# Kernel optimization log

Hardware: AMD Instinct MI355X
Metric: run time of the kernel (lower is better)

Reference implementation:

```python
import jax, jax.numpy as jnp
import numpy as np

GROUP_SIZE = 64

def _dequant(wq, scale, zero):
    # HQQ groupwise dequant: W = (Wq - zero) * scale, groups along input dim.
    out_dim, in_dim = wq.shape
    g = in_dim // GROUP_SIZE
    w = (wq.astype(jnp.float32).reshape(out_dim, g, GROUP_SIZE) - zero[:, :, None]) * scale[:, :, None]
    return w.reshape(out_dim, in_dim)

def setup_inputs() -> dict:
    key = jax.random.key(0)
    ks = jax.random.split(key, 10)
    T, H, I = 256, 4096, 14336
    G1, G2 = H // GROUP_SIZE, I // GROUP_SIZE  # 64, 224
    x = jax.random.normal(ks[0], (T, H), dtype=jnp.float32)
    w1_q = jax.random.randint(ks[1], (I, H), 0, 16, dtype=jnp.int32)
    w1_scale = jax.random.uniform(ks[2], (I, G1), dtype=jnp.float32) * 0.02
    w1_zero = jax.random.uniform(ks[3], (I, G1), dtype=jnp.float32) * 8.0
    w3_q = jax.random.randint(ks[4], (I, H), 0, 16, dtype=jnp.int32)
    w3_scale = jax.random.uniform(ks[5], (I, G1), dtype=jnp.float32) * 0.02
    w3_zero = jax.random.uniform(ks[6], (I, G1), dtype=jnp.float32) * 8.0
    w2_q = jax.random.randint(ks[7], (H, I), 0, 16, dtype=jnp.int32)
    w2_scale = jax.random.uniform(ks[8], (H, G2), dtype=jnp.float32) * 0.02
    w2_zero = jax.random.uniform(ks[9], (H, G2), dtype=jnp.float32) * 8.0
    return {"x": x, "w1_q": w1_q, "w1_scale": w1_scale, "w1_zero": w1_zero,
            "w3_q": w3_q, "w3_scale": w3_scale, "w3_zero": w3_zero,
            "w2_q": w2_q, "w2_scale": w2_scale, "w2_zero": w2_zero}

def reference(x, w1_q, w1_scale, w1_zero, w3_q, w3_scale, w3_zero, w2_q, w2_scale, w2_zero):
    w1 = _dequant(w1_q, w1_scale, w1_zero)  # [I, H]
    w3 = _dequant(w3_q, w3_scale, w3_zero)  # [I, H]
    w2 = _dequant(w2_q, w2_scale, w2_zero)  # [H, I]
    gate = jax.nn.silu(jnp.einsum('th,ih->ti', x, w1))  # [T, I]
    up = jnp.einsum('th,ih->ti', x, w3)                 # [T, I]
    return jnp.einsum('ti,hi->th', gate * up, w2)       # [T, H]
```

## Files before the change

### kernel.cpp

```cpp
#include <hip/hip_runtime.h>
#include <cstdint>
#include <cstddef>

#define T_DIM 256
#define H_DIM 4096
#define I_DIM 14336

typedef __attribute__((ext_vector_type(8))) short s8v;
typedef __attribute__((ext_vector_type(4))) float f4v;

static constexpr size_t XS_BYTES   = (size_t)T_DIM * H_DIM * 2;
static constexpr size_t ACT_OFF    = XS_BYTES;
static constexpr size_t ACT_BYTES  = (size_t)T_DIM * I_DIM * 2;
static constexpr size_t PART_OFF   = ACT_OFF + ACT_BYTES;
static constexpr size_t PART_BYTES = 8ull * T_DIM * H_DIM * 4;
static constexpr size_t WS_NEEDED  = PART_OFF + PART_BYTES;

__device__ __forceinline__ unsigned short f2bf(float f) {
    unsigned u = __builtin_bit_cast(unsigned, f);
    u += 0x7fffu + ((u >> 16) & 1u);
    return (unsigned short)(u >> 16);
}

__device__ __forceinline__ void g2lds16(const void* g, void* l) {
    __builtin_amdgcn_global_load_lds(
        (const __attribute__((address_space(1))) unsigned int*)g,
        (__attribute__((address_space(3))) unsigned int*)l,
        16, 0, 0);
}

__device__ __forceinline__ s8v dq8(const int4 qa, const int4 qb, float s, float ns) {
    union { unsigned short u[8]; s8v v; } r;
    r.u[0] = f2bf(fmaf((float)qa.x, s, ns));
    r.u[1] = f2bf(fmaf((float)qa.y, s, ns));
    r.u[2] = f2bf(fmaf((float)qa.z, s, ns));
    r.u[3] = f2bf(fmaf((float)qa.w, s, ns));
    r.u[4] = f2bf(fmaf((float)qb.x, s, ns));
    r.u[5] = f2bf(fmaf((float)qb.y, s, ns));
    r.u[6] = f2bf(fmaf((float)qb.z, s, ns));
    r.u[7] = f2bf(fmaf((float)qb.w, s, ns));
    return r.v;
}

__global__ __launch_bounds__(256) void k_prep(const float* __restrict__ x,
                                              unsigned short* __restrict__ xs) {
    int gs   = blockIdx.x * 256 + threadIdx.x;
    int kt   = gs >> 11;
    int rem  = gs & 2047;
    int row  = rem >> 3;
    int slot = rem & 7;
    const float* xp = x + (size_t)row * H_DIM + kt * 64 + slot * 8;
    float4 a = *(const float4*)xp;
    float4 b = *(const float4*)(xp + 4);
    union { unsigned short u[8]; s8v v; } r;
    r.u[0] = f2bf(a.x); r.u[1] = f2bf(a.y); r.u[2] = f2bf(a.z); r.u[3] = f2bf(a.w);
    r.u[4] = f2bf(b.x); r.u[5] = f2bf(b.y); r.u[6] = f2bf(b.z); r.u[7] = f2bf(b.w);
    size_t di = (size_t)kt * 16384 + (size_t)row * 64 + (size_t)((slot ^ (row & 7)) * 8);
    *(s8v*)(xs + di) = r.v;
}

__global__ __launch_bounds__(512, 2) void k_gemm1(
    const int* __restrict__ w1q, const float* __restrict__ w1s, const float* __restrict__ w1z,
    const int* __restrict__ w3q, const float* __restrict__ w3s, const float* __restrict__ w3z,
    const unsigned short* __restrict__ xs, unsigned short* __restrict__ act)
{
    __shared__ unsigned char lds[49152];
    const int tid  = threadIdx.x;
    const int blk  = blockIdx.x;
    const int n0   = blk * 64;
    const int wid  = tid >> 6;
    const int lane = tid & 63;
    const int wr   = wid >> 1;
    const int wc   = wid & 1;
    const int lr   = lane & 15;
    const int lkb  = lane >> 4;
    const int aswz = (lr & 7) << 4;

    const int srow  = tid >> 3;
    const int sslot = tid & 7;
    const size_t grow = (size_t)(n0 + srow) * H_DIM + (size_t)sslot * 8;
    const int wbyte = srow * 128 + ((sslot * 16) ^ ((srow & 7) << 4));
    const float* s1p = w1s + (size_t)(n0 + srow) * 64;
    const float* z1p = w1z + (size_t)(n0 + srow) * 64;
    const float* s3p = w3s + (size_t)(n0 + srow) * 64;
    const float* z3p = w3z + (size_t)(n0 + srow) * 64;

    f4v accg[4][2], accu[4][2];
    const f4v fz = {0.f, 0.f, 0.f, 0.f};
    #pragma unroll
    for (int i = 0; i < 4; ++i)
        #pragma unroll
        for (int j = 0; j < 2; ++j) { accg[i][j] = fz; accu[i][j] = fz; }

    const unsigned char* xsb = (const unsigned char*)xs;

    for (int kt = 0; kt < 64; ++kt) {
        {
            const unsigned char* gsrc = xsb + (size_t)kt * 32768 + (size_t)wid * 1024
                                            + (size_t)lane * 16;
            unsigned char* ldst = lds + wid * 1024;
            #pragma unroll
            for (int j = 0; j < 4; ++j)
                g2lds16(gsrc + j * 8192, ldst + j * 8192);
        }
        {
            const int4* p1 = (const int4*)(w1q + grow + (size_t)kt * 64);
            const int4* p3 = (const int4*)(w3q + grow + (size_t)kt * 64);
            int4 q1a = p1[0], q1b = p1[1];
            int4 q3a = p3[0], q3b = p3[1];
            float s1 = s1p[kt]; float ns1 = -z1p[kt] * s1;
            float s3 = s3p[kt]; float ns3 = -z3p[kt] * s3;
            *(s8v*)(lds + 32768 + wbyte) = dq8(q1a, q1b, s1, ns1);
            *(s8v*)(lds + 40960 + wbyte) = dq8(q3a, q3b, s3, ns3);
        }
        __syncthreads();
        #pragma unroll
        for (int kf = 0; kf < 2; ++kf) {
            const int kb = (kf * 64 + lkb * 16) ^ aswz;
            s8v a[4];
            #pragma unroll
            for (int mf = 0; mf < 4; ++mf)
                a[mf] = *(const s8v*)(lds + (wr * 64 + mf * 16 + lr) * 128 + kb);
            s8v b1[2], b3[2];
            #pragma unroll
            for (int nf = 0; nf < 2; ++nf) {
                const int rbo = (wc * 32 + nf * 16 + lr) * 128 + kb;
                b1[nf] = *(const s8v*)(lds + 32768 + rbo);
                b3[nf] = *(const s8v*)(lds + 40960 + rbo);
            }
            #pragma unroll
            for (int mf = 0; mf < 4; ++mf)
                #pragma unroll
                for (int nf = 0; nf < 2; ++nf) {
                    accg[mf][nf] = __builtin_amdgcn_mfma_f32_16x16x32_bf16(a[mf], b1[nf], accg[mf][nf], 0, 0, 0);
                    accu[mf][nf] = __builtin_amdgcn_mfma_f32_16x16x32_bf16(a[mf], b3[nf], accu[mf][nf], 0, 0, 0);
                }
        }
        __syncthreads();
    }

    unsigned char* actb = (unsigned char*)act + (size_t)blk * 32768;
    #pragma unroll
    for (int mf = 0; mf < 4; ++mf)
        #pragma unroll
        for (int nf = 0; nf < 2; ++nf)
            #pragma unroll
            for (int r = 0; r < 4; ++r) {
                const int m  = wr * 64 + mf * 16 + lkb * 4 + r;
                const int nl = wc * 32 + nf * 16 + lr;
                float g = accg[mf][nf][r];
                float u = accu[mf][nf][r];
                float sg = g / (1.0f + __expf(-g));
                *(unsigned short*)(actb + ((m * 128 + nl * 2) ^ ((m & 7) << 4))) = f2bf(sg * u);
            }
}

template<bool ATOMIC>
__global__ __launch_bounds__(512, 2) void k_gemm2(
    const int* __restrict__ w2q, const float* __restrict__ w2s, const float* __restrict__ w2z,
    const unsigned short* __restrict__ act, float* __restrict__ outp)
{
    __shared__ unsigned char lds[49152];
    const int tid  = threadIdx.x;
    const int nb   = blockIdx.x & 31;
    const int kc   = blockIdx.x >> 5;
    const int n0   = nb * 128;
    const int wid  = tid >> 6;
    const int lane = tid & 63;
    const int wr   = wid >> 2;
    const int wc   = wid & 3;
    const int lr   = lane & 15;
    const int lkb  = lane >> 4;
    const int aswz = (lr & 7) << 4;

    const int srow = tid >> 2;
    const int ss2  = (tid & 3) * 2;
    const size_t grow = (size_t)(n0 + srow) * I_DIM + (size_t)ss2 * 8;
    const int wb0 = srow * 128 + ((ss2 * 16)       ^ ((srow & 7) << 4));
    const int wb1 = srow * 128 + (((ss2 + 1) * 16) ^ ((srow & 7) << 4));
    const float* s2p = w2s + (size_t)(n0 + srow) * 224;
    const float* z2p = w2z + (size_t)(n0 + srow) * 224;

    f4v acc[8][2];
    const f4v fz = {0.f, 0.f, 0.f, 0.f};
    #pragma unroll
    for (int i = 0; i < 8; ++i) { acc[i][0] = fz; acc[i][1] = fz; }

    const unsigned char* actb = (const unsigned char*)act;
    const int kt0 = kc * 28;

    for (int kk = 0; kk < 28; ++kk) {
        const int kt = kt0 + kk;
        {
            const unsigned char* gsrc = actb + (size_t)kt * 32768 + (size_t)wid * 1024
                                             + (size_t)lane * 16;
            unsigned char* ldst = lds + wid * 1024;
            #pragma unroll
            for (int j = 0; j < 4; ++j)
                g2lds16(gsrc + j * 8192, ldst + j * 8192);
        }
        {
            const int4* p2 = (const int4*)(w2q + grow + (size_t)kt * 64);
            int4 qa = p2[0], qb = p2[1], qc = p2[2], qd = p2[3];
            float s2 = s2p[kt]; float ns2 = -z2p[kt] * s2;
            *(s8v*)(lds + 32768 + wb0) = dq8(qa, qb, s2, ns2);
            *(s8v*)(lds + 32768 + wb1) = dq8(qc, qd, s2, ns2);
        }
        __syncthreads();
        #pragma unroll
        for (int kf = 0; kf < 2; ++kf) {
            const int kb = (kf * 64 + lkb * 16) ^ aswz;
            s8v b2[2];
            #pragma unroll
            for (int nf = 0; nf < 2; ++nf)
                b2[nf] = *(const s8v*)(lds + 32768 + (wc * 32 + nf * 16 + lr) * 128 + kb);
            #pragma unroll
            for (int mf = 0; mf < 8; ++mf) {
                s8v a = *(const s8v*)(lds + (wr * 128 + mf * 16 + lr) * 128 + kb);
                acc[mf][0] = __builtin_amdgcn_mfma_f32_16x16x32_bf16(a, b2[0], acc[mf][0], 0, 0, 0);
                acc[mf][1] = __builtin_amdgcn_mfma_f32_16x16x32_bf16(a, b2[1], acc[mf][1], 0, 0, 0);
            }
        }
        __syncthreads();
    }

    float* pout = outp + (ATOMIC ? 0 : (size_t)kc * ((size_t)T_DIM * H_DIM));
    #pragma unroll
    for (int mf = 0; mf < 8; ++mf)
        #pragma unroll
        for (int nf = 0; nf < 2; ++nf)
            #pragma unroll
            for (int r = 0; r < 4; ++r) {
                const int m = wr * 128 + mf * 16 + lkb * 4 + r;
                const int n = n0 + wc * 32 + nf * 16 + lr;
                if (ATOMIC) atomicAdd(&outp[(size_t)m * H_DIM + n], acc[mf][nf][r]);
                else        pout[(size_t)m * H_DIM + n] = acc[mf][nf][r];
            }
}

__global__ __launch_bounds__(256) void k_reduce(const f4v* __restrict__ p,
                                                f4v* __restrict__ o) {
    int i = blockIdx.x * 256 + threadIdx.x;
    f4v s = p[i];
    #pragma unroll
    for (int c = 1; c < 8; ++c) s += p[(size_t)c * 262144 + i];
    o[i] = s;
}

__global__ __launch_bounds__(256) void k_zero(f4v* __restrict__ o) {
    o[blockIdx.x * 256 + threadIdx.x] = (f4v){0.f, 0.f, 0.f, 0.f};
}

extern "C" void kernel_launch(void* const* d_in, const int* in_sizes, int n_in,
                              void* d_out, int out_size, void* d_ws, size_t ws_size,
                              hipStream_t stream) {
    const float* x   = (const float*)d_in[0];
    const int*   w1q = (const int*)  d_in[1];
    const float* w1s = (const float*)d_in[2];
    const float* w1z = (const float*)d_in[3];
    const int*   w3q = (const int*)  d_in[4];
    const float* w3s = (const float*)d_in[5];
    const float* w3z = (const float*)d_in[6];
    const int*   w2q = (const int*)  d_in[7];
    const float* w2s = (const float*)d_in[8];
    const float* w2z = (const float*)d_in[9];
    float* outp = (float*)d_out;

    unsigned short* xs  = (unsigned short*)d_ws;
    unsigned short* act = (unsigned short*)((char*)d_ws + ACT_OFF);
    float*          prt = (float*)((char*)d_ws + PART_OFF);
    const bool partials = (ws_size >= WS_NEEDED);

    k_prep<<<512, 256, 0, stream>>>(x, xs);
    k_gemm1<<<224, 512, 0, stream>>>(w1q, w1s, w1z, w3q, w3s, w3z, xs, act);
    if (partials) {
        k_gemm2<false><<<256, 512, 0, stream>>>(w2q, w2s, w2z, act, prt);
        k_reduce<<<1024, 256, 0, stream>>>((const f4v*)prt, (f4v*)outp);
    } else {
        k_zero<<<1024, 256, 0, stream>>>((f4v*)outp);
        k_gemm2<true><<<256, 512, 0, stream>>>(w2q, w2s, w2z, act, outp);
    }
}
```

Measured before the change: 284.9 us.

## Replace LDS-tiled GEMMs with register-streamed direct-load MFMA kernels

Both GEMM kernels are rewritten so that each wave streams int32 weights from global memory into registers, dequantises them in registers with packed bf16 conversion, and feeds MFMA directly. The LDS staging, block barriers and split-K partial-sum reduction are removed. Activations are pre-laid-out in MFMA fragment order so A operands come straight from global memory. A new prep kernel transposes and prefolds the scales and zeros into float2 pairs. The aim is to remove LDS and sync overhead and keep the weight stream saturating bandwidth. The risk is lower data reuse per block and a GEMM2 with only 256 blocks and no split-K, which may underfill the GPU over its long K loop.

```diff
diff --git a/kernel.cpp b/kernel.cpp
--- a/kernel.cpp
+++ b/kernel.cpp
@@ -9,12 +9,14 @@
 typedef __attribute__((ext_vector_type(8))) short s8v;
 typedef __attribute__((ext_vector_type(4))) float f4v;
 
-static constexpr size_t XS_BYTES   = (size_t)T_DIM * H_DIM * 2;
-static constexpr size_t ACT_OFF    = XS_BYTES;
-static constexpr size_t ACT_BYTES  = (size_t)T_DIM * I_DIM * 2;
-static constexpr size_t PART_OFF   = ACT_OFF + ACT_BYTES;
-static constexpr size_t PART_BYTES = 8ull * T_DIM * H_DIM * 4;
-static constexpr size_t WS_NEEDED  = PART_OFF + PART_BYTES;
+static constexpr size_t XS_OFF   = 0;
+static constexpr size_t ACT_OFF  = (size_t)T_DIM * H_DIM * 2;
+static constexpr size_t ACT_BYTES= (size_t)T_DIM * I_DIM * 2;
+static constexpr size_t G1_OFF   = ACT_OFF + ACT_BYTES;
+static constexpr size_t G3_OFF   = G1_OFF + (size_t)64 * I_DIM * 8;
+static constexpr size_t G2_OFF   = G3_OFF + (size_t)64 * I_DIM * 8;
+static constexpr size_t WS_NEED  = G2_OFF + (size_t)224 * H_DIM * 8;
+static constexpr size_t WS_MIN   = G1_OFF;
 
 __device__ __forceinline__ unsigned short f2bf(float f) {
     unsigned u = __builtin_bit_cast(unsigned, f);
@@ -22,233 +24,234 @@
     return (unsigned short)(u >> 16);
 }
 
-__device__ __forceinline__ void g2lds16(const void* g, void* l) {
-    __builtin_amdgcn_global_load_lds(
-        (const __attribute__((address_space(1))) unsigned int*)g,
-        (__attribute__((address_space(3))) unsigned int*)l,
-        16, 0, 0);
-}
-
-__device__ __forceinline__ s8v dq8(const int4 qa, const int4 qb, float s, float ns) {
-    union { unsigned short u[8]; s8v v; } r;
-    r.u[0] = f2bf(fmaf((float)qa.x, s, ns));
-    r.u[1] = f2bf(fmaf((float)qa.y, s, ns));
-    r.u[2] = f2bf(fmaf((float)qa.z, s, ns));
-    r.u[3] = f2bf(fmaf((float)qa.w, s, ns));
-    r.u[4] = f2bf(fmaf((float)qb.x, s, ns));
-    r.u[5] = f2bf(fmaf((float)qb.y, s, ns));
-    r.u[6] = f2bf(fmaf((float)qb.z, s, ns));
-    r.u[7] = f2bf(fmaf((float)qb.w, s, ns));
-    return r.v;
+__device__ __forceinline__ s8v dq8f(const int4 qa, const int4 qb, float s, float ns) {
+    float f0 = fmaf((float)qa.x, s, ns), f1 = fmaf((float)qa.y, s, ns);
+    float f2 = fmaf((float)qa.z, s, ns), f3 = fmaf((float)qa.w, s, ns);
+    float f4 = fmaf((float)qb.x, s, ns), f5 = fmaf((float)qb.y, s, ns);
+    float f6 = fmaf((float)qb.z, s, ns), f7 = fmaf((float)qb.w, s, ns);
+    unsigned r0, r1, r2, r3;
+    asm("v_cvt_pk_bf16_f32 %0, %1, %2" : "=v"(r0) : "v"(f0), "v"(f1));
+    asm("v_cvt_pk_bf16_f32 %0, %1, %2" : "=v"(r1) : "v"(f2), "v"(f3));
+    asm("v_cvt_pk_bf16_f32 %0, %1, %2" : "=v"(r2) : "v"(f4), "v"(f5));
+    asm("v_cvt_pk_bf16_f32 %0, %1, %2" : "=v"(r3) : "v"(f6), "v"(f7));
+    union { unsigned u[4]; s8v v; } o;
+    o.u[0] = r0; o.u[1] = r1; o.u[2] = r2; o.u[3] = r3;
+    return o.v;
 }
 
 __global__ __launch_bounds__(256) void k_prep(const float* __restrict__ x,
                                               unsigned short* __restrict__ xs) {
-    int gs   = blockIdx.x * 256 + threadIdx.x;
-    int kt   = gs >> 11;
-    int rem  = gs & 2047;
-    int row  = rem >> 3;
-    int slot = rem & 7;
-    const float* xp = x + (size_t)row * H_DIM + kt * 64 + slot * 8;
+    int t = blockIdx.x * 256 + threadIdx.x;
+    int l = t & 63, f = t >> 6;
+    int msub = f & 15, ksub = f >> 4;
+    int m = msub * 16 + (l & 15);
+    int k = ksub * 32 + (l >> 4) * 8;
+    const float* xp = x + (size_t)m * H_DIM + k;
     float4 a = *(const float4*)xp;
     float4 b = *(const float4*)(xp + 4);
     union { unsigned short u[8]; s8v v; } r;
     r.u[0] = f2bf(a.x); r.u[1] = f2bf(a.y); r.u[2] = f2bf(a.z); r.u[3] = f2bf(a.w);
     r.u[4] = f2bf(b.x); r.u[5] = f2bf(b.y); r.u[6] = f2bf(b.z); r.u[7] = f2bf(b.w);
-    size_t di = (size_t)kt * 16384 + (size_t)row * 64 + (size_t)((slot ^ (row & 7)) * 8);
-    *(s8v*)(xs + di) = r.v;
-}
-
-__global__ __launch_bounds__(512, 2) void k_gemm1(
-    const int* __restrict__ w1q, const float* __restrict__ w1s, const float* __restrict__ w1z,
-    const int* __restrict__ w3q, const float* __restrict__ w3s, const float* __restrict__ w3z,
-    const unsigned short* __restrict__ xs, unsigned short* __restrict__ act)
+    *((s8v*)xs + t) = r.v;
+}
+
+__global__ __launch_bounds__(256) void t_prep(
+    const float* __restrict__ w1s, const float* __restrict__ w1z,
+    const float* __restrict__ w3s, const float* __restrict__ w3z,
+    const float* __restrict__ w2s, const float* __restrict__ w2z,
+    float2* __restrict__ g1, float2* __restrict__ g3, float2* __restrict__ g2)
 {
-    __shared__ unsigned char lds[49152];
-    const int tid  = threadIdx.x;
-    const int blk  = blockIdx.x;
-    const int n0   = blk * 64;
-    const int wid  = tid >> 6;
-    const int lane = tid & 63;
-    const int wr   = wid >> 1;
-    const int wc   = wid & 1;
-    const int lr   = lane & 15;
-    const int lkb  = lane >> 4;
-    const int aswz = (lr & 7) << 4;
-
-    const int srow  = tid >> 3;
-    const int sslot = tid & 7;
-    const size_t grow = (size_t)(n0 + srow) * H_DIM + (size_t)sslot * 8;
-    const int wbyte = srow * 128 + ((sslot * 16) ^ ((srow & 7) << 4));
-    const float* s1p = w1s + (size_t)(n0 + srow) * 64;
-    const float* z1p = w1z + (size_t)(n0 + srow) * 64;
-    const float* s3p = w3s + (size_t)(n0 + srow) * 64;
-    const float* z3p = w3z + (size_t)(n0 + srow) * 64;
-
-    f4v accg[4][2], accu[4][2];
+    int aid = blockIdx.x / 3584;
+    int r   = (blockIdx.x - aid * 3584) * 256 + threadIdx.x;
+    if (aid < 2) {
+        int n = r % I_DIM, g = r / I_DIM;
+        const float* S = aid ? w3s : w1s;
+        const float* Z = aid ? w3z : w1z;
+        float s = S[(size_t)n * 64 + g], z = Z[(size_t)n * 64 + g];
+        (aid ? g3 : g1)[r] = make_float2(s, z * s);
+    } else {
+        int n = r & (H_DIM - 1), g = r >> 12;
+        float s = w2s[(size_t)n * 224 + g], z = w2z[(size_t)n * 224 + g];
+        g2[r] = make_float2(s, z * s);
+    }
+}
+
+template<bool TR>
+__global__ __launch_bounds__(128, 2) void k_gemm1(
+    const int* __restrict__ w1q, const int* __restrict__ w3q,
+    const float* __restrict__ w1s, const float* __restrict__ w1z,
+    const float* __restrict__ w3s, const float* __restrict__ w3z,
+    const float2* __restrict__ g1, const float2* __restrict__ g3,
+    const unsigned char* __restrict__ xs, unsigned short* __restrict__ act)
+{
+    const int tid = threadIdx.x, wid = tid >> 6, l = tid & 63;
+    const int m  = blockIdx.x & 3, nb = blockIdx.x >> 2;
+    const int n0 = nb * 64 + wid * 32;
+    const int lr = l & 15, lk = l >> 4;
+    const int rA = n0 + lr, rB = n0 + 16 + lr;
+
+    const int* p1A = w1q + (size_t)rA * H_DIM + lk * 8;
+    const int* p1B = w1q + (size_t)rB * H_DIM + lk * 8;
+    const int* p3A = w3q + (size_t)rA * H_DIM + lk * 8;
+    const int* p3B = w3q + (size_t)rB * H_DIM + lk * 8;
+    const unsigned char* xp = xs + (size_t)(m * 4) * 1024 + (size_t)l * 16;
+
+    f4v ag[4][2], au[4][2];
     const f4v fz = {0.f, 0.f, 0.f, 0.f};
     #pragma unroll
-    for (int i = 0; i < 4; ++i)
-        #pragma unroll
-        for (int j = 0; j < 2; ++j) { accg[i][j] = fz; accu[i][j] = fz; }
-
-    const unsigned char* xsb = (const unsigned char*)xs;
-
-    for (int kt = 0; kt < 64; ++kt) {
-        {
-            const unsigned char* gsrc = xsb + (size_t)kt * 32768 + (size_t)wid * 1024
-                                            + (size_t)lane * 16;
-            unsigned char* ldst = lds + wid * 1024;
-            #pragma unroll
-            for (int j = 0; j < 4; ++j)
-                g2lds16(gsrc + j * 8192, ldst + j * 8192);
-        }
-        {
-            const int4* p1 = (const int4*)(w1q + grow + (size_t)kt * 64);
-            const int4* p3 = (const int4*)(w3q + grow + (size_t)kt * 64);
-            int4 q1a = p1[0], q1b = p1[1];
-            int4 q3a = p3[0], q3b = p3[1];
-            float s1 = s1p[kt]; float ns1 = -z1p[kt] * s1;
-            float s3 = s3p[kt]; float ns3 = -z3p[kt] * s3;
-            *(s8v*)(lds + 32768 + wbyte) = dq8(q1a, q1b, s1, ns1);
-            *(s8v*)(lds + 40960 + wbyte) = dq8(q3a, q3b, s3, ns3);
-        }
-        __syncthreads();
-        #pragma unroll
-        for (int kf = 0; kf < 2; ++kf) {
-            const int kb = (kf * 64 + lkb * 16) ^ aswz;
-            s8v a[4];
-            #pragma unroll
-            for (int mf = 0; mf < 4; ++mf)
-                a[mf] = *(const s8v*)(lds + (wr * 64 + mf * 16 + lr) * 128 + kb);
-            s8v b1[2], b3[2];
-            #pragma unroll
-            for (int nf = 0; nf < 2; ++nf) {
-                const int rbo = (wc * 32 + nf * 16 + lr) * 128 + kb;
-                b1[nf] = *(const s8v*)(lds + 32768 + rbo);
-                b3[nf] = *(const s8v*)(lds + 40960 + rbo);
-            }
-            #pragma unroll
-            for (int mf = 0; mf < 4; ++mf)
-                #pragma unroll
-                for (int nf = 0; nf < 2; ++nf) {
-                    accg[mf][nf] = __builtin_amdgcn_mfma_f32_16x16x32_bf16(a[mf], b1[nf], accg[mf][nf], 0, 0, 0);
-                    accu[mf][nf] = __builtin_amdgcn_mfma_f32_16x16x32_bf16(a[mf], b3[nf], accu[mf][nf], 0, 0, 0);
-                }
-        }
-        __syncthreads();
-    }
-
-    unsigned char* actb = (unsigned char*)act + (size_t)blk * 32768;
+    for (int i = 0; i < 4; ++i) { ag[i][0] = fz; ag[i][1] = fz; au[i][0] = fz; au[i][1] = fz; }
+
+    auto ldsc = [&](int g, int row) -> float2 {
+        if constexpr (TR) {
+            return row < 16 ? g1[(size_t)g * I_DIM + (row == 0 ? rA : rB)]
+                            : g3[(size_t)g * I_DIM + (row == 16 ? rA : rB)];
+        } else {
+            const float* S = row < 16 ? w1s : w3s;
+            const float* Z = row < 16 ? w1z : w3z;
+            int rr = (row & 15) == 0 ? rA : rB;
+            float s = S[(size_t)rr * 64 + g], z = Z[(size_t)rr * 64 + g];
+            return make_float2(s, z * s);
+        }
+    };
+
+    int4 c1Aa = *(const int4*)p1A, c1Ab = *(const int4*)(p1A + 4);
+    int4 c1Ba = *(const int4*)p1B, c1Bb = *(const int4*)(p1B + 4);
+    int4 c3Aa = *(const int4*)p3A, c3Ab = *(const int4*)(p3A + 4);
+    int4 c3Ba = *(const int4*)p3B, c3Bb = *(const int4*)(p3B + 4);
+    float2 s1A = ldsc(0, 0), s1B = ldsc(0, 1), s3A = ldsc(0, 16), s3B = ldsc(0, 17);
+
+    for (int g = 0; g < 64; ++g) {
+        const int gn = g < 63 ? g + 1 : 63;
+        float2 t1A = ldsc(gn, 0), t1B = ldsc(gn, 1), t3A = ldsc(gn, 16), t3B = ldsc(gn, 17);
+        #pragma unroll
+        for (int h = 0; h < 2; ++h) {
+            const int t  = g * 2 + h;
+            const int tn = t < 127 ? t + 1 : 127;
+            int4 n1Aa = *(const int4*)(p1A + tn * 32), n1Ab = *(const int4*)(p1A + tn * 32 + 4);
+            int4 n1Ba = *(const int4*)(p1B + tn * 32), n1Bb = *(const int4*)(p1B + tn * 32 + 4);
+            int4 n3Aa = *(const int4*)(p3A + tn * 32), n3Ab = *(const int4*)(p3A + tn * 32 + 4);
+            int4 n3Ba = *(const int4*)(p3B + tn * 32), n3Bb = *(const int4*)(p3B + tn * 32 + 4);
+            const unsigned char* xq = xp + (size_t)t * 16384;
+            s8v a0 = *(const s8v*)(xq);
+            s8v a1 = *(const s8v*)(xq + 1024);
+            s8v a2 = *(const s8v*)(xq + 2048);
+            s8v a3 = *(const s8v*)(xq + 3072);
+            s8v b1A = dq8f(c1Aa, c1Ab, s1A.x, -s1A.y);
+            s8v b1B = dq8f(c1Ba, c1Bb, s1B.x, -s1B.y);
+            s8v b3A = dq8f(c3Aa, c3Ab, s3A.x, -s3A.y);
+            s8v b3B = dq8f(c3Ba, c3Bb, s3B.x, -s3B.y);
+            ag[0][0] = __builtin_amdgcn_mfma_f32_16x16x32_bf16(a0, b1A, ag[0][0], 0, 0, 0);
+            ag[1][0] = __builtin_amdgcn_mfma_f32_16x16x32_bf16(a1, b1A, ag[1][0], 0, 0, 0);
+            ag[2][0] = __builtin_amdgcn_mfma_f32_16x16x32_bf16(a2, b1A, ag[2][0], 0, 0, 0);
+            ag[3][0] = __builtin_amdgcn_mfma_f32_16x16x32_bf16(a3, b1A, ag[3][0], 0, 0, 0);
+            ag[0][1] = __builtin_amdgcn_mfma_f32_16x16x32_bf16(a0, b1B, ag[0][1], 0, 0, 0);
+            ag[1][1] = __builtin_amdgcn_mfma_f32_16x16x32_bf16(a1, b1B, ag[1][1], 0, 0, 0);
+            ag[2][1] = __builtin_amdgcn_mfma_f32_16x16x32_bf16(a2, b1B, ag[2][1], 0, 0, 0);
+            ag[3][1] = __builtin_amdgcn_mfma_f32_16x16x32_bf16(a3, b1B, ag[3][1], 0, 0, 0);
+            au[0][0] = __builtin_amdgcn_mfma_f32_16x16x32_bf16(a0, b3A, au[0][0], 0, 0, 0);
+            au[1][0] = __builtin_amdgcn_mfma_f32_16x16x32_bf16(a1, b3A, au[1][0], 0, 0, 0);
+            au[2][0] = __builtin_amdgcn_mfma_f32_16x16x32_bf16(a2, b3A, au[2][0], 0, 0, 0);
+            au[3][0] = __builtin_amdgcn_mfma_f32_16x16x32_bf16(a3, b3A, au[3][0], 0, 0, 0);
+            au[0][1] = __builtin_amdgcn_mfma_f32_16x16x32_bf16(a0, b3B, au[0][1], 0, 0, 0);
+            au[1][1] = __builtin_amdgcn_mfma_f32_16x16x32_bf16(a1, b3B, au[1][1], 0, 0, 0);
+            au[2][1] = __builtin_amdgcn_mfma_f32_16x16x32_bf16(a2, b3B, au[2][1], 0, 0, 0);
+            au[3][1] = __builtin_amdgcn_mfma_f32_16x16x32_bf16(a3, b3B, au[3][1], 0, 0, 0);
+            c1Aa = n1Aa; c1Ab = n1Ab; c1Ba = n1Ba; c1Bb = n1Bb;
+            c3Aa = n3Aa; c3Ab = n3Ab; c3Ba = n3Ba; c3Bb = n3Bb;
+        }
+        s1A = t1A; s1B = t1B; s3A = t3A; s3B = t3B;
+    }
+
+    unsigned char* ab = (unsigned char*)act;
     #pragma unroll
-    for (int mf = 0; mf < 4; ++mf)
+    for (int mf = 0; mf < 4; ++mf) {
+        const int msub = m * 4 + mf;
         #pragma unroll
         for (int nf = 0; nf < 2; ++nf)
             #pragma unroll
             for (int r = 0; r < 4; ++r) {
-                const int m  = wr * 64 + mf * 16 + lkb * 4 + r;
-                const int nl = wc * 32 + nf * 16 + lr;
-                float g = accg[mf][nf][r];
-                float u = accu[mf][nf][r];
-                float sg = g / (1.0f + __expf(-g));
-                *(unsigned short*)(actb + ((m * 128 + nl * 2) ^ ((m & 7) << 4))) = f2bf(sg * u);
+                const int N  = n0 + nf * 16 + lr;
+                const int l2 = (lk * 4 + r) + (((N >> 3) & 3) << 4);
+                float gg = ag[mf][nf][r], uu = au[mf][nf][r];
+                float sg = gg / (1.0f + __expf(-gg));
+                *(unsigned short*)(ab + ((size_t)((N >> 5) * 16 + msub) << 10)
+                                      + l2 * 16 + (N & 7) * 2) = f2bf(sg * uu);
             }
-}
-
-template<bool ATOMIC>
-__global__ __launch_bounds__(512, 2) void k_gemm2(
-    const int* __restrict__ w2q, const float* __restrict__ w2s, const float* __restrict__ w2z,
-    const unsigned short* __restrict__ act, float* __restrict__ outp)
+    }
+}
+
+template<bool TR>
+__global__ __launch_bounds__(256) void k_gemm2(
+    const int* __restrict__ w2q,
+    const float* __restrict__ w2s, const float* __restrict__ w2z,
+    const float2* __restrict__ g2,
+    const unsigned char* __restrict__ act, float* __restrict__ outp)
 {
-    __shared__ unsigned char lds[49152];
-    const int tid  = threadIdx.x;
-    const int nb   = blockIdx.x & 31;
-    const int kc   = blockIdx.x >> 5;
-    const int n0   = nb * 128;
-    const int wid  = tid >> 6;
-    const int lane = tid & 63;
-    const int wr   = wid >> 2;
-    const int wc   = wid & 3;
-    const int lr   = lane & 15;
-    const int lkb  = lane >> 4;
-    const int aswz = (lr & 7) << 4;
-
-    const int srow = tid >> 2;
-    const int ss2  = (tid & 3) * 2;
-    const size_t grow = (size_t)(n0 + srow) * I_DIM + (size_t)ss2 * 8;
-    const int wb0 = srow * 128 + ((ss2 * 16)       ^ ((srow & 7) << 4));
-    const int wb1 = srow * 128 + (((ss2 + 1) * 16) ^ ((srow & 7) << 4));
-    const float* s2p = w2s + (size_t)(n0 + srow) * 224;
-    const float* z2p = w2z + (size_t)(n0 + srow) * 224;
-
-    f4v acc[8][2];
+    const int tid = threadIdx.x, wid = tid >> 6, l = tid & 63;
+    const int m  = blockIdx.x & 7, nb = blockIdx.x >> 3;
+    const int n0 = nb * 128 + wid * 32;
+    const int m0 = m * 32;
+    const int lr = l & 15, lk = l >> 4;
+    const int rA = n0 + lr, rB = n0 + 16 + lr;
+
+    const int* pA = w2q + (size_t)rA * I_DIM + lk * 8;
+    const int* pB = w2q + (size_t)rB * I_DIM + lk * 8;
+    const unsigned char* xp = act + (size_t)(m * 2) * 1024 + (size_t)l * 16;
+
+    f4v acc[2][2];
     const f4v fz = {0.f, 0.f, 0.f, 0.f};
+    acc[0][0] = fz; acc[0][1] = fz; acc[1][0] = fz; acc[1][1] = fz;
+
+    auto ldsc = [&](int g, int which) -> float2 {
+        if constexpr (TR) {
+            return g2[(size_t)g * H_DIM + (which ? rB : rA)];
+        } else {
+            int rr = which ? rB : rA;
+            float s = w2s[(size_t)rr * 224 + g], z = w2z[(size_t)rr * 224 + g];
+            return make_float2(s, z * s);
+        }
+    };
+
+    int4 cAa = *(const int4*)pA, cAb = *(const int4*)(pA + 4);
+    int4 cBa = *(const int4*)pB, cBb = *(const int4*)(pB + 4);
+    int4 dAa = *(const int4*)(pA + 32), dAb = *(const int4*)(pA + 36);
+    int4 dBa = *(const int4*)(pB + 32), dBb = *(const int4*)(pB + 36);
+    float2 sA = ldsc(0, 0), sB = ldsc(0, 1);
+
+    for (int g = 0; g < 224; ++g) {
+        const int gn = g < 223 ? g + 1 : 223;
+        float2 tA = ldsc(gn, 0), tB = ldsc(gn, 1);
+        #pragma unroll
+        for (int h = 0; h < 2; ++h) {
+            const int t  = g * 2 + h;
+            const int tn = t < 446 ? t + 2 : 447;
+            int4 nAa = *(const int4*)(pA + tn * 32), nAb = *(const int4*)(pA + tn * 32 + 4);
+            int4 nBa = *(const int4*)(pB + tn * 32), nBb = *(const int4*)(pB + tn * 32 + 4);
+            const unsigned char* xq = xp + (size_t)t * 16384;
+            s8v a0 = *(const s8v*)(xq);
+            s8v a1 = *(const s8v*)(xq + 1024);
+            s8v bA = dq8f(cAa, cAb, sA.x, -sA.y);
+            s8v bB = dq8f(cBa, cBb, sB.x, -sB.y);
+            acc[0][0] = __builtin_amdgcn_mfma_f32_16x16x32_bf16(a0, bA, acc[0][0], 0, 0, 0);
+            acc[1][0] = __builtin_amdgcn_mfma_f32_16x16x32_bf16(a1, bA, acc[1][0], 0, 0, 0);
+            acc[0][1] = __builtin_amdgcn_mfma_f32_16x16x32_bf16(a0, bB, acc[0][1], 0, 0, 0);
+            acc[1][1] = __builtin_amdgcn_mfma_f32_16x16x32_bf16(a1, bB, acc[1][1], 0, 0, 0);
+            cAa = dAa; cAb = dAb; cBa = dBa; cBb = dBb;
+            dAa = nAa; dAb = nAb; dBa = nBa; dBb = nBb;
+        }
+        sA = tA; sB = tB;
+    }
+
     #pragma unroll
-    for (int i = 0; i < 8; ++i) { acc[i][0] = fz; acc[i][1] = fz; }
-
-    const unsigned char* actb = (const unsigned char*)act;
-    const int kt0 = kc * 28;
-
-    for (int kk = 0; kk < 28; ++kk) {
-        const int kt = kt0 + kk;
-        {
-            const unsigned char* gsrc = actb + (size_t)kt * 32768 + (size_t)wid * 1024
-                                             + (size_t)lane * 16;
-            unsigned char* ldst = lds + wid * 1024;
-            #pragma unroll
-            for (int j = 0; j < 4; ++j)
-                g2lds16(gsrc + j * 8192, ldst + j * 8192);
-        }
-        {
-            const int4* p2 = (const int4*)(w2q + grow + (size_t)kt * 64);
-            int4 qa = p2[0], qb = p2[1], qc = p2[2], qd = p2[3];
-            float s2 = s2p[kt]; float ns2 = -z2p[kt] * s2;
-            *(s8v*)(lds + 32768 + wb0) = dq8(qa, qb, s2, ns2);
-            *(s8v*)(lds + 32768 + wb1) = dq8(qc, qd, s2, ns2);
-        }
-        __syncthreads();
-        #pragma unroll
-        for (int kf = 0; kf < 2; ++kf) {
-            const int kb = (kf * 64 + lkb * 16) ^ aswz;
-            s8v b2[2];
-            #pragma unroll
-            for (int nf = 0; nf < 2; ++nf)
-                b2[nf] = *(const s8v*)(lds + 32768 + (wc * 32 + nf * 16 + lr) * 128 + kb);
-            #pragma unroll
-            for (int mf = 0; mf < 8; ++mf) {
-                s8v a = *(const s8v*)(lds + (wr * 128 + mf * 16 + lr) * 128 + kb);
-                acc[mf][0] = __builtin_amdgcn_mfma_f32_16x16x32_bf16(a, b2[0], acc[mf][0], 0, 0, 0);
-                acc[mf][1] = __builtin_amdgcn_mfma_f32_16x16x32_bf16(a, b2[1], acc[mf][1], 0, 0, 0);
-            }
-        }
-        __syncthreads();
-    }
-
-    float* pout = outp + (ATOMIC ? 0 : (size_t)kc * ((size_t)T_DIM * H_DIM));
-    #pragma unroll
-    for (int mf = 0; mf < 8; ++mf)
+    for (int mf = 0; mf < 2; ++mf)
         #pragma unroll
         for (int nf = 0; nf < 2; ++nf)
             #pragma unroll
             for (int r = 0; r < 4; ++r) {
-                const int m = wr * 128 + mf * 16 + lkb * 4 + r;
-                const int n = n0 + wc * 32 + nf * 16 + lr;
-                if (ATOMIC) atomicAdd(&outp[(size_t)m * H_DIM + n], acc[mf][nf][r]);
-                else        pout[(size_t)m * H_DIM + n] = acc[mf][nf][r];
+                const int M = m0 + mf * 16 + lk * 4 + r;
+                const int N = n0 + nf * 16 + lr;
+                outp[(size_t)M * H_DIM + N] = acc[mf][nf][r];
             }
-}
-
-__global__ __launch_bounds__(256) void k_reduce(const f4v* __restrict__ p,
-                                                f4v* __restrict__ o) {
-    int i = blockIdx.x * 256 + threadIdx.x;
-    f4v s = p[i];
-    #pragma unroll
-    for (int c = 1; c < 8; ++c) s += p[(size_t)c * 262144 + i];
-    o[i] = s;
-}
-
-__global__ __launch_bounds__(256) void k_zero(f4v* __restrict__ o) {
-    o[blockIdx.x * 256 + threadIdx.x] = (f4v){0.f, 0.f, 0.f, 0.f};
 }
 
 extern "C" void kernel_launch(void* const* d_in, const int* in_sizes, int n_in,
@@ -266,18 +269,24 @@
     const float* w2z = (const float*)d_in[9];
     float* outp = (float*)d_out;
 
-    unsigned short* xs  = (unsigned short*)d_ws;
+    unsigned short* xs  = (unsigned short*)((char*)d_ws + XS_OFF);
     unsigned short* act = (unsigned short*)((char*)d_ws + ACT_OFF);
-    float*          prt = (float*)((char*)d_ws + PART_OFF);
-    const bool partials = (ws_size >= WS_NEEDED);
+    float2* g1 = (float2*)((char*)d_ws + G1_OFF);
+    float2* g3 = (float2*)((char*)d_ws + G3_OFF);
+    float2* g2 = (float2*)((char*)d_ws + G2_OFF);
+    const bool tr = (ws_size >= WS_NEED);
 
     k_prep<<<512, 256, 0, stream>>>(x, xs);
-    k_gemm1<<<224, 512, 0, stream>>>(w1q, w1s, w1z, w3q, w3s, w3z, xs, act);
-    if (partials) {
-        k_gemm2<false><<<256, 512, 0, stream>>>(w2q, w2s, w2z, act, prt);
-        k_reduce<<<1024, 256, 0, stream>>>((const f4v*)prt, (f4v*)outp);
+    if (tr) {
+        t_prep<<<10752, 256, 0, stream>>>(w1s, w1z, w3s, w3z, w2s, w2z, g1, g3, g2);
+        k_gemm1<true><<<896, 128, 0, stream>>>(w1q, w3q, w1s, w1z, w3s, w3z, g1, g3,
+                                               (const unsigned char*)xs, act);
+        k_gemm2<true><<<256, 256, 0, stream>>>(w2q, w2s, w2z, g2,
+                                               (const unsigned char*)act, outp);
     } else {
-        k_zero<<<1024, 256, 0, stream>>>((f4v*)outp);
-        k_gemm2<true><<<256, 512, 0, stream>>>(w2q, w2s, w2z, act, outp);
-    }
-}
+        k_gemm1<false><<<896, 128, 0, stream>>>(w1q, w3q, w1s, w1z, w3s, w3z, g1, g3,
+                                                (const unsigned char*)xs, act);
+        k_gemm2<false><<<256, 256, 0, stream>>>(w2q, w2s, w2z, g2,
+                                                (const unsigned char*)act, outp);
+    }
+}
```

New measurement: 881.6 us. +209.5%, slower.
